# Optimization experiments

Hardware: AMD Instinct MI355X
Metric: run time of the kernel (lower is better)

## Reference

```python
import jax, jax.numpy as jnp
import numpy as np

B, N, C_IN, C_OUT, E_DIM = 16, 1024, 64, 64, 4


def setup_inputs() -> dict:
    key = jax.random.key(0)
    ks = jax.random.split(key, 7)
    x = jax.random.normal(ks[0], (B, N, C_IN), dtype=jnp.float32)
    adj = jax.random.uniform(ks[1], (B, N, N), dtype=jnp.float32)
    edge_attr = jax.random.randint(ks[2], (B, N, N, 1), 0, E_DIM, dtype=jnp.int32)
    scale = 1.0 / np.sqrt(C_IN)
    W_rel = jax.random.normal(ks[3], (C_IN, C_OUT), dtype=jnp.float32) * scale
    b_rel = jax.random.normal(ks[4], (C_OUT,), dtype=jnp.float32) * scale
    W_root = jax.random.normal(ks[5], (C_IN, C_OUT), dtype=jnp.float32) * scale
    w_edge = jax.random.normal(ks[6], (E_DIM,), dtype=jnp.float32)
    return {"x": x, "adj": adj, "edge_attr": edge_attr,
            "W_rel": W_rel, "b_rel": b_rel, "W_root": W_root, "w_edge": w_edge}


def reference(x, adj, edge_attr, W_rel, b_rel, W_root, w_edge):
    # one_hot(edge_attr) @ w_edge == gather of w_edge by edge type (same math,
    # avoids materializing the B x N x N x E_DIM one-hot tensor).
    e = w_edge[edge_attr[..., 0]]            # [B, N, N]
    adj_w = adj * e                           # weighted adjacency
    out = jnp.matmul(adj_w, x)                # [B, N, C_IN] aggregation (aggr='add')
    out = jnp.matmul(out, W_rel) + b_rel      # lin_rel
    out = out + jnp.matmul(x, W_root)         # lin_root (no bias)
    return out
```

## Files before the change

### kernel.cpp

```cpp
#include <hip/hip_runtime.h>

#define BB 16
#define NN 1024
#define CC 64

typedef __attribute__((ext_vector_type(8))) short short8;
typedef __attribute__((ext_vector_type(4))) float f32x4;
typedef __attribute__((ext_vector_type(4))) int   i32x4;

__device__ __forceinline__ unsigned short bf16_rne(float f) {
    unsigned u = __float_as_uint(f);
    u += 0x7fffu + ((u >> 16) & 1u);
    return (unsigned short)(u >> 16);
}

extern "C" __global__ __launch_bounds__(256)
void precompute(const float* __restrict__ x, const float* __restrict__ W_rel,
                const float* __restrict__ W_root, const float* __restrict__ b_rel,
                unsigned short* __restrict__ xw_sw, float* __restrict__ out)
{
    __shared__ float wrel_s[64 * 64];
    __shared__ float wroot_s[64 * 64];
    __shared__ float x_s[16 * 68];

    const int t = threadIdx.x;
    #pragma unroll
    for (int k = 0; k < 4; ++k) {
        int i4 = t + 256 * k;
        ((float4*)wrel_s)[i4]  = ((const float4*)W_rel)[i4];
        ((float4*)wroot_s)[i4] = ((const float4*)W_root)[i4];
    }
    const int row0 = blockIdx.x * 16;
    {
        int r = t >> 4, c4 = t & 15;
        *(float4*)(x_s + r * 68 + c4 * 4) = ((const float4*)(x + (size_t)(row0 + r) * CC))[c4];
    }
    __syncthreads();

    const int c4 = t & 15;
    const int r  = t >> 4;
    float aw0 = 0.f, aw1 = 0.f, aw2 = 0.f, aw3 = 0.f;
    float ar0 = 0.f, ar1 = 0.f, ar2 = 0.f, ar3 = 0.f;
    const float* xrow = x_s + r * 68;
    #pragma unroll 8
    for (int k = 0; k < 64; ++k) {
        float xv = xrow[k];
        float4 wv = ((const float4*)(wrel_s  + k * 64))[c4];
        float4 rv = ((const float4*)(wroot_s + k * 64))[c4];
        aw0 += xv * wv.x; aw1 += xv * wv.y; aw2 += xv * wv.z; aw3 += xv * wv.w;
        ar0 += xv * rv.x; ar1 += xv * rv.y; ar2 += xv * rv.z; ar3 += xv * rv.w;
    }

    const int row_g = row0 + r;
    {
        const float4 bv = ((const float4*)b_rel)[c4];
        ((float4*)out)[(size_t)row_g * 16 + c4] =
            make_float4(ar0 + bv.x, ar1 + bv.y, ar2 + bv.z, ar3 + bv.w);
    }
    {
        const int b = row_g >> 10;
        const int k = row_g & 1023;
        const int kb = k >> 5;
        const int qk = (k >> 3) & 3;
        const int j  = k & 7;
        const int c  = 4 * c4;
        const int n0 = c >> 4;
        const int n  = c & 15;
        size_t off = ((size_t)b << 16) + (size_t)((kb * 4 + n0) << 9)
                   + (size_t)((n + (qk << 4)) << 3) + j;
        xw_sw[off]      = bf16_rne(aw0);
        xw_sw[off + 8]  = bf16_rne(aw1);
        xw_sw[off + 16] = bf16_rne(aw2);
        xw_sw[off + 24] = bf16_rne(aw3);
    }
}

extern "C" __global__ __launch_bounds__(256, 2)
void gnn_mfma(const float* __restrict__ adj, const int* __restrict__ ea,
              const float* __restrict__ w_edge,
              const unsigned short* __restrict__ xw_sw,
              float* __restrict__ out)
{
    __shared__ __align__(16) char lds[65536];

    const int t     = threadIdx.x;
    const int mtile = blockIdx.x & 31;
    const int b     = blockIdx.x >> 5;
    const int row0  = mtile << 5;

    const float w0 = w_edge[0], w1 = w_edge[1], w2 = w_edge[2], w3 = w_edge[3];
    const float d1 = w1 - w0;
    const float d2 = w2 - 2.f * w1 + w0;
    const float d3 = w3 - 3.f * w2 + 3.f * w1 - w0;
    const float c3 = d3 * (1.f / 6.f);
    const float c2 = 0.5f * d2 - 0.5f * d3;
    const float c1 = d1 - 0.5f * d2 + (1.f / 3.f) * d3;
    const float c0 = w0;

#define WSEL(ev) __builtin_fmaf(__builtin_fmaf(__builtin_fmaf(c3, (float)(ev), c2), (float)(ev), c1), (float)(ev), c0)

    const size_t gbase = ((size_t)b << 20) + ((size_t)row0 << 10);
    const float4* A4 = (const float4*)(adj + gbase);
    const i32x4*  E4 = (const i32x4*)(ea + gbase);

    const int kb_t   = t >> 3;
    const int q_t    = (t >> 1) & 3;
    const int X_t    = ((kb_t & 3) << 2) | q_t;
    const int wbase  = (kb_t << 10) + (q_t << 8) + ((t & 1) << 3);

    float4 aa[8]; i32x4 ee[8];
    #pragma unroll
    for (int d = 0; d < 8; ++d) { aa[d] = A4[d * 256 + t]; ee[d] = E4[d * 256 + t]; }

    #pragma unroll
    for (int i = 0; i < 32; ++i) {
        float4 av = aa[i & 7];
        i32x4  ev = ee[i & 7];
        if (i < 24) {
            aa[i & 7] = A4[(i + 8) * 256 + t];
            ee[i & 7] = E4[(i + 8) * 256 + t];
        }
        float p0 = av.x * WSEL(ev[0]);
        float p1 = av.y * WSEL(ev[1]);
        float p2 = av.z * WSEL(ev[2]);
        float p3 = av.w * WSEL(ev[3]);
        unsigned u0 = __builtin_amdgcn_perm(__float_as_uint(p1), __float_as_uint(p0), 0x07060302u);
        unsigned u1 = __builtin_amdgcn_perm(__float_as_uint(p3), __float_as_uint(p2), 0x07060302u);
        const int m  = i & 15;
        const int mh = i >> 4;
        const int addr = (mh << 15) + wbase + ((m ^ X_t) << 4);
        *(uint2*)(lds + addr) = make_uint2(u0, u1);
    }
    __syncthreads();

    const int w    = t >> 6;
    const int lane = t & 63;
    const int m    = lane & 15;
    const int q    = lane >> 4;
    const int wm   = w >> 1;
    const int wn   = w & 1;

    const unsigned short* xwb = xw_sw + ((size_t)b << 16)
                              + ((size_t)(wn * 2) << 9) + ((size_t)lane << 3);
    const char* abase = lds + (wm << 15) + (q << 8);

    f32x4 acc0 = {0.f, 0.f, 0.f, 0.f};
    f32x4 acc1 = acc0;

    #pragma unroll
    for (int kb = 0; kb < 32; ++kb) {
        const int X = ((kb & 3) << 2) | q;
        short8 af = *(const short8*)(abase + (kb << 10) + ((m ^ X) << 4));
        const unsigned short* xq = xwb + ((size_t)kb << 11);
        short8 bf0 = *(const short8*)(xq);
        short8 bf1 = *(const short8*)(xq + 512);
        acc0 = __builtin_amdgcn_mfma_f32_16x16x32_bf16(af, bf0, acc0, 0, 0, 0);
        acc1 = __builtin_amdgcn_mfma_f32_16x16x32_bf16(af, bf1, acc1, 0, 0, 0);
    }
#undef WSEL

    const size_t R0 = ((size_t)b << 10) + row0 + (wm << 4) + (q << 2);
    float* ob = out + (R0 << 6) + (wn << 5) + m;
    #pragma unroll
    for (int rg = 0; rg < 4; ++rg) {
        ob[rg * 64]      += acc0[rg];
        ob[rg * 64 + 16] += acc1[rg];
    }
}

extern "C" void kernel_launch(void* const* d_in, const int* in_sizes, int n_in,
                              void* d_out, int out_size, void* d_ws, size_t ws_size,
                              hipStream_t stream) {
    const float* x      = (const float*)d_in[0];
    const float* adj    = (const float*)d_in[1];
    const int*   ea     = (const int*)  d_in[2];
    const float* W_rel  = (const float*)d_in[3];
    const float* b_rel  = (const float*)d_in[4];
    const float* W_root = (const float*)d_in[5];
    const float* w_edge = (const float*)d_in[6];
    float* out = (float*)d_out;

    unsigned short* xw_sw = (unsigned short*)d_ws;

    precompute<<<BB * NN / 16, 256, 0, stream>>>(x, W_rel, W_root, b_rel, xw_sw, out);
    gnn_mfma<<<BB * (NN / 32), 256, 0, stream>>>(adj, ea, w_edge, xw_sw, out);
}
```

Before: 173.8 us.

## Halve row tile to 16 rows per block and use nontemporal adj/edge loads

The GEMM kernel now processes 16 adjacency rows per block instead of 32. That doubles the grid, halves LDS to 32 KB and raises the occupancy target to 4 blocks per CU. Each wave now computes a single 16x16 output tile instead of two, so every wave reads a different slice of xw and shares the same A tile. The streamed adj and edge_attr reads switch to nontemporal loads so they stay out of the cache. The aim is more parallelism and latency hiding for this bandwidth-bound stream, at the cost of reloading xw_sw from L2 more often and issuing fewer MFMAs per LDS load.

```diff
diff --git a/kernel.cpp b/kernel.cpp
--- a/kernel.cpp
+++ b/kernel.cpp
@@ -75,18 +75,18 @@
     }
 }
 
-extern "C" __global__ __launch_bounds__(256, 2)
+extern "C" __global__ __launch_bounds__(256, 4)
 void gnn_mfma(const float* __restrict__ adj, const int* __restrict__ ea,
               const float* __restrict__ w_edge,
               const unsigned short* __restrict__ xw_sw,
               float* __restrict__ out)
 {
-    __shared__ __align__(16) char lds[65536];
+    __shared__ __align__(16) char lds[32768];
 
     const int t     = threadIdx.x;
-    const int mtile = blockIdx.x & 31;
-    const int b     = blockIdx.x >> 5;
-    const int row0  = mtile << 5;
+    const int mtile = blockIdx.x & 63;
+    const int b     = blockIdx.x >> 6;
+    const int row0  = mtile << 4;
 
     const float w0 = w_edge[0], w1 = w_edge[1], w2 = w_edge[2], w3 = w_edge[3];
     const float d1 = w1 - w0;
@@ -100,71 +100,65 @@
 #define WSEL(ev) __builtin_fmaf(__builtin_fmaf(__builtin_fmaf(c3, (float)(ev), c2), (float)(ev), c1), (float)(ev), c0)
 
     const size_t gbase = ((size_t)b << 20) + ((size_t)row0 << 10);
-    const float4* A4 = (const float4*)(adj + gbase);
-    const i32x4*  E4 = (const i32x4*)(ea + gbase);
+    const f32x4* A4 = (const f32x4*)(adj + gbase);
+    const i32x4* E4 = (const i32x4*)(ea + gbase);
 
     const int kb_t   = t >> 3;
     const int q_t    = (t >> 1) & 3;
     const int X_t    = ((kb_t & 3) << 2) | q_t;
     const int wbase  = (kb_t << 10) + (q_t << 8) + ((t & 1) << 3);
 
-    float4 aa[8]; i32x4 ee[8];
+    f32x4 aa[8]; i32x4 ee[8];
     #pragma unroll
-    for (int d = 0; d < 8; ++d) { aa[d] = A4[d * 256 + t]; ee[d] = E4[d * 256 + t]; }
+    for (int d = 0; d < 8; ++d) {
+        aa[d] = __builtin_nontemporal_load(&A4[d * 256 + t]);
+        ee[d] = __builtin_nontemporal_load(&E4[d * 256 + t]);
+    }
 
     #pragma unroll
-    for (int i = 0; i < 32; ++i) {
-        float4 av = aa[i & 7];
-        i32x4  ev = ee[i & 7];
-        if (i < 24) {
-            aa[i & 7] = A4[(i + 8) * 256 + t];
-            ee[i & 7] = E4[(i + 8) * 256 + t];
+    for (int i = 0; i < 16; ++i) {
+        f32x4 av = aa[i & 7];
+        i32x4 ev = ee[i & 7];
+        if (i < 8) {
+            aa[i & 7] = __builtin_nontemporal_load(&A4[(i + 8) * 256 + t]);
+            ee[i & 7] = __builtin_nontemporal_load(&E4[(i + 8) * 256 + t]);
         }
-        float p0 = av.x * WSEL(ev[0]);
-        float p1 = av.y * WSEL(ev[1]);
-        float p2 = av.z * WSEL(ev[2]);
-        float p3 = av.w * WSEL(ev[3]);
+        float p0 = av[0] * WSEL(ev[0]);
+        float p1 = av[1] * WSEL(ev[1]);
+        float p2 = av[2] * WSEL(ev[2]);
+        float p3 = av[3] * WSEL(ev[3]);
         unsigned u0 = __builtin_amdgcn_perm(__float_as_uint(p1), __float_as_uint(p0), 0x07060302u);
         unsigned u1 = __builtin_amdgcn_perm(__float_as_uint(p3), __float_as_uint(p2), 0x07060302u);
-        const int m  = i & 15;
-        const int mh = i >> 4;
-        const int addr = (mh << 15) + wbase + ((m ^ X_t) << 4);
+        const int m = i;
+        const int addr = wbase + ((m ^ X_t) << 4);
         *(uint2*)(lds + addr) = make_uint2(u0, u1);
     }
     __syncthreads();
 
-    const int w    = t >> 6;
+    const int wn   = t >> 6;
     const int lane = t & 63;
     const int m    = lane & 15;
     const int q    = lane >> 4;
-    const int wm   = w >> 1;
-    const int wn   = w & 1;
 
     const unsigned short* xwb = xw_sw + ((size_t)b << 16)
-                              + ((size_t)(wn * 2) << 9) + ((size_t)lane << 3);
-    const char* abase = lds + (wm << 15) + (q << 8);
+                              + ((size_t)wn << 9) + ((size_t)lane << 3);
+    const char* abase = lds + (q << 8);
 
     f32x4 acc0 = {0.f, 0.f, 0.f, 0.f};
-    f32x4 acc1 = acc0;
 
     #pragma unroll
     for (int kb = 0; kb < 32; ++kb) {
         const int X = ((kb & 3) << 2) | q;
         short8 af = *(const short8*)(abase + (kb << 10) + ((m ^ X) << 4));
-        const unsigned short* xq = xwb + ((size_t)kb << 11);
-        short8 bf0 = *(const short8*)(xq);
-        short8 bf1 = *(const short8*)(xq + 512);
-        acc0 = __builtin_amdgcn_mfma_f32_16x16x32_bf16(af, bf0, acc0, 0, 0, 0);
-        acc1 = __builtin_amdgcn_mfma_f32_16x16x32_bf16(af, bf1, acc1, 0, 0, 0);
+        short8 bf = *(const short8*)(xwb + ((size_t)kb << 11));
+        acc0 = __builtin_amdgcn_mfma_f32_16x16x32_bf16(af, bf, acc0, 0, 0, 0);
     }
 #undef WSEL
 
-    const size_t R0 = ((size_t)b << 10) + row0 + (wm << 4) + (q << 2);
-    float* ob = out + (R0 << 6) + (wn << 5) + m;
+    float* ob = out + ((((size_t)b << 10) + row0 + (q << 2)) << 6) + (wn << 4) + m;
     #pragma unroll
     for (int rg = 0; rg < 4; ++rg) {
-        ob[rg * 64]      += acc0[rg];
-        ob[rg * 64 + 16] += acc1[rg];
+        ob[rg * 64] += acc0[rg];
     }
 }
 
@@ -183,5 +177,5 @@
     unsigned short* xw_sw = (unsigned short*)d_ws;
 
     precompute<<<BB * NN / 16, 256, 0, stream>>>(x, W_rel, W_root, b_rel, xw_sw, out);
-    gnn_mfma<<<BB * (NN / 32), 256, 0, stream>>>(adj, ea, w_edge, xw_sw, out);
+    gnn_mfma<<<BB * (NN / 16), 256, 0, stream>>>(adj, ea, w_edge, xw_sw, out);
 }
```

After: 164.9 us. -5.1%, faster.
